# Performance work log

Hardware: AMD Instinct MI355X
Metric: run time of the kernel (lower is better)

The kernel has to match this reference:

```python
import jax, jax.numpy as jnp
import numpy as np

N = 131072       # active sparse sites (fixed)
C_IN = 256       # FPN input channels
HID = 512        # CONV_HEAD_DIM
K = 9            # 3x3 kernel taps
LAYERS = 8       # NUM_STACKED_CONVS
GROUPS = 32      # GroupNorm groups (detectron2 default)
EPS = 1e-5


def _build_rulebook(rng):
    # Sample sparse occupancy over 64 ROIs of 64x64, build 3x3 neighbor map.
    B, H, W = 64, 64, 64
    mask = rng.random((B, H, W)) < 0.60
    coords = np.argwhere(mask)[:N]          # [N,3] (b,y,x), fixed N
    assert coords.shape[0] == N
    grid = -np.ones((B, H + 2, W + 2), np.int32)  # padded, -1 = inactive
    grid[coords[:, 0], coords[:, 1] + 1, coords[:, 2] + 1] = np.arange(N, dtype=np.int32)
    offs = [(dy, dx) for dy in (-1, 0, 1) for dx in (-1, 0, 1)]
    nbr = np.stack(
        [grid[coords[:, 0], coords[:, 1] + 1 + dy, coords[:, 2] + 1 + dx] for dy, dx in offs],
        axis=1,
    )  # [N,9], -1 where neighbor inactive (submanifold: output sites == input sites)
    return nbr


def setup_inputs() -> dict:
    rng = np.random.default_rng(0)
    nbr = _build_rulebook(rng)
    key = jax.random.key(0)
    k0, k1, k2, k3, k4 = jax.random.split(key, 5)
    features = jax.random.normal(k0, (N, C_IN), jnp.float32)
    w0 = jax.random.normal(k1, (K, C_IN, HID), jnp.float32) * (1.0 / np.sqrt(K * C_IN))
    w_rest = jax.random.normal(k2, (LAYERS - 1, K, HID, HID), jnp.float32) * (1.0 / np.sqrt(K * HID))
    gamma = 1.0 + 0.1 * jax.random.normal(k3, (LAYERS, HID), jnp.float32)
    beta = 0.1 * jax.random.normal(k4, (LAYERS, HID), jnp.float32)
    return {
        "features": features,
        "nbr_idx": jnp.asarray(nbr),
        "w0": w0,
        "w_rest": w_rest,
        "gamma": gamma,
        "beta": beta,
    }


def _subm_conv(x, nbr_idx, w):
    # gather-GEMM-scatter submanifold conv: x [N,Cin], nbr_idx [N,K], w [K,Cin,Cout]
    n = x.shape[0]
    xp = jnp.concatenate([x, jnp.zeros((1, x.shape[1]), x.dtype)], axis=0)  # zero row for -1
    idx = jnp.where(nbr_idx < 0, n, nbr_idx)
    out = jnp.zeros((n, w.shape[2]), x.dtype)
    for k in range(K):  # fixed small loop over kernel taps
        out = out + xp[idx[:, k]] @ w[k]
    return out


def _group_norm(x, g, b):
    # per-point GroupNorm over channel groups: x [N,C]
    n, c = x.shape
    xg = x.reshape(n, GROUPS, c // GROUPS)
    mu = jnp.mean(xg, axis=-1, keepdims=True)
    var = jnp.var(xg, axis=-1, keepdims=True)
    xg = (xg - mu) * jax.lax.rsqrt(var + EPS)
    return xg.reshape(n, c) * g + b


def reference(features, nbr_idx, w0, w_rest, gamma, beta):
    x = jax.nn.relu(_group_norm(_subm_conv(features, nbr_idx, w0), gamma[0], beta[0]))
    for i in range(LAYERS - 1):
        x = jax.nn.relu(_group_norm(_subm_conv(x, nbr_idx, w_rest[i]), gamma[i + 1], beta[i + 1]))
    return x
```

## Files before the change

kernel.cpp:

```cpp
#include <hip/hip_runtime.h>
#include <stdint.h>

#define N_SITES 131072
#define CIN0 256
#define HID 512
#define KTAPS 9
#define NLAYERS 8

typedef __bf16 bf16x8 __attribute__((ext_vector_type(8)));
typedef float f32x4 __attribute__((ext_vector_type(4)));

__device__ __forceinline__ unsigned short f2bf(float f) {
    union { float f; unsigned u; } v; v.f = f;
    return (unsigned short)((v.u + 0x7fffu + ((v.u >> 16) & 1u)) >> 16);
}


__global__ void cvt_features_kernel(const float* __restrict__ in, unsigned short* __restrict__ out) {
    int t = blockIdx.x * 256 + threadIdx.x;
    const float4* p = (const float4*)in + 2 * (size_t)t;
    float4 a = p[0], b = p[1];
    uint4 o;
    o.x = f2bf(a.x) | ((unsigned)f2bf(a.y) << 16);
    o.y = f2bf(a.z) | ((unsigned)f2bf(a.w) << 16);
    o.z = f2bf(b.x) | ((unsigned)f2bf(b.y) << 16);
    o.w = f2bf(b.z) | ((unsigned)f2bf(b.w) << 16);
    ((uint4*)out)[t] = o;
}

__global__ void zero_rows_kernel(unsigned short* __restrict__ xf, unsigned short* __restrict__ xo) {
    int t = threadIdx.x;
    xf[(size_t)N_SITES * 512 + t] = 0;
    xf[(size_t)N_SITES * 512 + 256 + t] = 0;
    xo[(size_t)N_SITES * 256 + t] = 0;
    xo[(size_t)N_SITES * 512 + t] = 0;
    xo[(size_t)N_SITES * 512 + 256 + t] = 0;
}

__global__ void transpose_w_kernel(const float* __restrict__ in, unsigned short* __restrict__ out, int cin) {
    __shared__ float tile[32][33];
    int m = blockIdx.z;
    int nb = blockIdx.x * 32;
    int cb = blockIdx.y * 32;
    int tx = threadIdx.x, ty = threadIdx.y;
    const float* src = in + (size_t)m * cin * HID;
    unsigned short* dst = out + (size_t)m * HID * cin;
#pragma unroll
    for (int j = 0; j < 4; ++j) {
        int r = ty + 8 * j;
        tile[r][tx] = src[(size_t)(cb + r) * HID + nb + tx];
    }
    __syncthreads();
#pragma unroll
    for (int j = 0; j < 4; ++j) {
        int r = ty + 8 * j;
        dst[(size_t)(nb + r) * cin + cb + tx] = f2bf(tile[tx][r]);
    }
}


__device__ __forceinline__ void async16(const void* g, void* l) {
    __builtin_amdgcn_global_load_lds(
        (__attribute__((address_space(1))) unsigned int*)(g),
        (__attribute__((address_space(3))) unsigned int*)(l),
        16, 0, 0);
}

__global__ __launch_bounds__(256, 4) void subm_gemm_gn_kernel(
    const unsigned short* __restrict__ x,
    const int* __restrict__ nbr,
    const unsigned short* __restrict__ wt,
    const float* __restrict__ gamma,
    const float* __restrict__ beta,
    void* __restrict__ obuf,
    int cin, int write_bf16)
{
    __shared__ uint4 As[1024];
    __shared__ uint4 Bs[1024];

    const int tid = threadIdx.x;
    const int lane = tid & 63;
    const int wave = tid >> 6;

    const int b = (int)blockIdx.x;
    const int xcd = b & 7;
    const int slot = b >> 3;
    const int colbase = (xcd & 3) * 128;
    const int rowbase = ((xcd >> 2) * 512 + slot) * 128;

    const int wm = (wave >> 1) * 64;
    const int wn = (wave & 1) * 64;

    const int r0 = tid >> 3;
    const int cs = tid & 7;
    const int chunk = cs ^ (r0 & 7);
    const int ldsbase = tid & ~63;
    const int kiters = cin >> 6;

    const f32x4 zero4 = {0.f, 0.f, 0.f, 0.f};
    f32x4 acc[4][4];
#pragma unroll
    for (int i = 0; i < 4; ++i)
#pragma unroll
        for (int j = 0; j < 4; ++j)
            acc[i][j] = zero4;

    for (int tap = 0; tap < KTAPS; ++tap) {
        const unsigned short* arow[4];
#pragma unroll
        for (int i = 0; i < 4; ++i) {
            int idx = nbr[(size_t)(rowbase + r0 + 32 * i) * KTAPS + tap];
            if (idx < 0) idx = N_SITES;
            arow[i] = x + (size_t)idx * cin + chunk * 8;
        }
        const unsigned short* wbase = wt + ((size_t)tap * HID + colbase) * cin + chunk * 8;
        const unsigned short* brow[4];
#pragma unroll
        for (int i = 0; i < 4; ++i)
            brow[i] = wbase + (size_t)(r0 + 32 * i) * cin;

        for (int kk = 0; kk < kiters; ++kk) {
            const int ko = kk * 64;
            __syncthreads();
#pragma unroll
            for (int i = 0; i < 4; ++i) {
                async16(arow[i] + ko, &As[ldsbase + 256 * i]);
                async16(brow[i] + ko, &Bs[ldsbase + 256 * i]);
            }
            __syncthreads();

#pragma unroll
            for (int ks = 0; ks < 2; ++ks) {
                bf16x8 af[4], bfr[4];
#pragma unroll
                for (int f = 0; f < 4; ++f) {
                    int rl = wm + f * 16 + (lane & 15);
                    int ch = ks * 4 + (lane >> 4);
                    af[f]  = __builtin_bit_cast(bf16x8, As[rl * 8 + (ch ^ (rl & 7))]);
                    int cl = wn + f * 16 + (lane & 15);
                    bfr[f] = __builtin_bit_cast(bf16x8, Bs[cl * 8 + (ch ^ (cl & 7))]);
                }
#pragma unroll
                for (int i = 0; i < 4; ++i)
#pragma unroll
                    for (int j = 0; j < 4; ++j)
                        acc[i][j] = __builtin_amdgcn_mfma_f32_16x16x32_bf16(af[i], bfr[j], acc[i][j], 0, 0, 0);
            }
        }
    }

    float gv[4], bv[4];
#pragma unroll
    for (int j = 0; j < 4; ++j) {
        int gcol = colbase + wn + j * 16 + (lane & 15);
        gv[j] = gamma[gcol];
        bv[j] = beta[gcol];
    }

    unsigned short* bf_out = (unsigned short*)obuf;
    float* f_out = (float*)obuf;

#pragma unroll
    for (int i = 0; i < 4; ++i) {
        const int grow = rowbase + wm + i * 16 + (lane >> 4) * 4;
#pragma unroll
        for (int j = 0; j < 4; ++j) {
            const int gcol = colbase + wn + j * 16 + (lane & 15);
            f32x4 v = acc[i][j];
            f32x4 s = v;
            f32x4 q = v * v;
#pragma unroll
            for (int m = 1; m < 16; m <<= 1) {
#pragma unroll
                for (int r = 0; r < 4; ++r) {
                    s[r] += __shfl_xor(s[r], m);
                    q[r] += __shfl_xor(q[r], m);
                }
            }
            f32x4 y;
#pragma unroll
            for (int r = 0; r < 4; ++r) {
                float mu = s[r] * 0.0625f;
                float rstd = rsqrtf(q[r] * 0.0625f - mu * mu + 1e-5f);
                y[r] = fmaxf(0.f, (v[r] - mu) * rstd * gv[j] + bv[j]);
            }
            if (write_bf16) {
#pragma unroll
                for (int r = 0; r < 4; ++r)
                    bf_out[(size_t)(grow + r) * HID + gcol] = f2bf(y[r]);
            } else {
#pragma unroll
                for (int r = 0; r < 4; ++r)
                    f_out[(size_t)(grow + r) * HID + gcol] = y[r];
            }
        }
    }
}


extern "C" void kernel_launch(void* const* d_in, const int* in_sizes, int n_in,
                              void* d_out, int out_size, void* d_ws, size_t ws_size,
                              hipStream_t stream) {
    const float* features = (const float*)d_in[0];
    const int*   nbr      = (const int*)d_in[1];
    const float* w0       = (const float*)d_in[2];
    const float* w_rest   = (const float*)d_in[3];
    const float* gamma    = (const float*)d_in[4];
    const float* beta     = (const float*)d_in[5];

    unsigned short* xF = (unsigned short*)d_ws;
    size_t xbytes = (size_t)(N_SITES + 1) * HID * sizeof(unsigned short);
    unsigned short* w0t = (unsigned short*)((char*)d_ws + xbytes);
    size_t w0t_bytes = (size_t)KTAPS * HID * CIN0 * sizeof(unsigned short);
    unsigned short* wrt = (unsigned short*)((char*)d_ws + xbytes + w0t_bytes);
    unsigned short* xO = (unsigned short*)d_out;

    cvt_features_kernel<<<N_SITES * CIN0 / (256 * 8), 256, 0, stream>>>(features, xO);
    zero_rows_kernel<<<1, 256, 0, stream>>>(xF, xO);
    transpose_w_kernel<<<dim3(HID / 32, CIN0 / 32, KTAPS), dim3(32, 8), 0, stream>>>(w0, w0t, CIN0);
    transpose_w_kernel<<<dim3(HID / 32, HID / 32, (NLAYERS - 1) * KTAPS), dim3(32, 8), 0, stream>>>(w_rest, wrt, HID);

    for (int l = 0; l < NLAYERS; ++l) {
        const unsigned short* wt = (l == 0) ? w0t : wrt + (size_t)(l - 1) * KTAPS * HID * HID;
        int cin = (l == 0) ? CIN0 : HID;
        const unsigned short* xin = (l & 1) ? xF : xO;
        void* obuf = (l == NLAYERS - 1) ? d_out : (void*)((l & 1) ? xO : xF);
        subm_gemm_gn_kernel<<<(N_SITES / 128) * 4, 256, 0, stream>>>(
            xin, nbr, wt, gamma + (size_t)l * HID, beta + (size_t)l * HID,
            obuf, cin, (l < NLAYERS - 1) ? 1 : 0);
    }
}
```

Measured before the change: 5.314 ms.

## Use 256x256 tiles with double-buffered eight-phase MFMA pipeline and LDS epilogue

Replaces the 128x128-tile, single-buffered gather-GEMM kernel with a 512-thread, 256x256-tile kernel templated on input channels. Global-to-LDS async loads of the next k-slice are interleaved with MFMA phases under explicit vmcnt waits, barriers and s_setprio. The kernel caches neighbor indices in shared memory and routes the GroupNorm epilogue through LDS so stores are vectorized. This aims to hide gather latency and raise per-block data reuse. In exchange it uses more registers and LDS and lowers occupancy, which risks spills or fewer resident waves.

```diff
diff --git a/kernel.cpp b/kernel.cpp
--- a/kernel.cpp
+++ b/kernel.cpp
@@ -66,132 +66,240 @@
         16, 0, 0);
 }
 
-__global__ __launch_bounds__(256, 4) void subm_gemm_gn_kernel(
+#define BARRIER() do { asm volatile("" ::: "memory"); __builtin_amdgcn_s_barrier(); asm volatile("" ::: "memory"); } while (0)
+#define WAIT_LGKM0() asm volatile("s_waitcnt lgkmcnt(0)" ::: "memory")
+#define WAIT_VM4() asm volatile("s_waitcnt vmcnt(4)" ::: "memory")
+#define WAIT_VM0() asm volatile("s_waitcnt vmcnt(0)" ::: "memory")
+
+#define MFMA4(I, A, B0_, B1_, B2_, B3_) \
+    acc[I][0] = __builtin_amdgcn_mfma_f32_16x16x32_bf16(A, B0_, acc[I][0], 0, 0, 0); \
+    acc[I][1] = __builtin_amdgcn_mfma_f32_16x16x32_bf16(A, B1_, acc[I][1], 0, 0, 0); \
+    acc[I][2] = __builtin_amdgcn_mfma_f32_16x16x32_bf16(A, B2_, acc[I][2], 0, 0, 0); \
+    acc[I][3] = __builtin_amdgcn_mfma_f32_16x16x32_bf16(A, B3_, acc[I][3], 0, 0, 0);
+
+template<int CIN>
+__global__ __launch_bounds__(512, 2) void subm_gemm_gn_8ph(
     const unsigned short* __restrict__ x,
     const int* __restrict__ nbr,
     const unsigned short* __restrict__ wt,
     const float* __restrict__ gamma,
     const float* __restrict__ beta,
     void* __restrict__ obuf,
-    int cin, int write_bf16)
+    int write_bf16)
 {
-    __shared__ uint4 As[1024];
-    __shared__ uint4 Bs[1024];
+    constexpr int KK = CIN / 64;
+    __shared__ uint4 lds[8192];
+    __shared__ int nbrS[256 * KTAPS];
 
     const int tid = threadIdx.x;
     const int lane = tid & 63;
     const int wave = tid >> 6;
+    const int wm = (wave >> 2) * 128;
+    const int wn = (wave & 3) * 64;
 
     const int b = (int)blockIdx.x;
     const int xcd = b & 7;
     const int slot = b >> 3;
-    const int colbase = (xcd & 3) * 128;
-    const int rowbase = ((xcd >> 2) * 512 + slot) * 128;
-
-    const int wm = (wave >> 1) * 64;
-    const int wn = (wave & 1) * 64;
-
-    const int r0 = tid >> 3;
-    const int cs = tid & 7;
-    const int chunk = cs ^ (r0 & 7);
-    const int ldsbase = tid & ~63;
-    const int kiters = cin >> 6;
+    const int colbase = (xcd & 1) * 256;
+    const int rowbase = ((xcd >> 1) * 128 + slot) * 256;
+
+    const int srow = 2 * (tid >> 3) + ((tid >> 2) & 1);
+    const int scl = (tid & 3) ^ ((tid >> 3) & 3);
+    const int ldsw = tid & ~63;
+
+    for (int u = tid; u < 256 * KTAPS; u += 512) {
+        int v = nbr[(size_t)rowbase * KTAPS + u];
+        nbrS[u] = (v < 0) ? N_SITES : v;
+    }
+    __syncthreads();
 
     const f32x4 zero4 = {0.f, 0.f, 0.f, 0.f};
-    f32x4 acc[4][4];
-#pragma unroll
-    for (int i = 0; i < 4; ++i)
+    f32x4 acc[8][4];
+#pragma unroll
+    for (int i = 0; i < 8; ++i)
 #pragma unroll
         for (int j = 0; j < 4; ++j)
             acc[i][j] = zero4;
 
+    auto stageA = [&](int i0, int i1, int kkp, int kh, int buf) {
+        const unsigned short* g0 = x + (size_t)i0 * CIN + kkp * 64 + kh * 32 + scl * 8;
+        const unsigned short* g1 = x + (size_t)i1 * CIN + kkp * 64 + kh * 32 + scl * 8;
+        async16(g0, &lds[buf * 4096 + kh * 1024 + ldsw]);
+        async16(g1, &lds[buf * 4096 + kh * 1024 + 512 + ldsw]);
+    };
+    auto stageB = [&](int tp, int kkp, int kh, int buf) {
+        const unsigned short* g0 = wt + (size_t)(tp * HID + colbase + srow) * CIN + kkp * 64 + kh * 32 + scl * 8;
+        const unsigned short* g1 = wt + (size_t)(tp * HID + colbase + srow + 128) * CIN + kkp * 64 + kh * 32 + scl * 8;
+        async16(g0, &lds[buf * 4096 + 2048 + kh * 1024 + ldsw]);
+        async16(g1, &lds[buf * 4096 + 2048 + kh * 1024 + 512 + ldsw]);
+    };
+    auto rdA = [&](int i, int ks, int buf) {
+        int rl = wm + i * 16 + (lane & 15);
+        return __builtin_bit_cast(bf16x8,
+            lds[buf * 4096 + ks * 1024 + (rl >> 1) * 8 + (rl & 1) * 4 + ((lane >> 4) ^ ((rl >> 1) & 3))]);
+    };
+    auto rdB = [&](int j, int ks, int buf) {
+        int rn = wn + j * 16 + (lane & 15);
+        return __builtin_bit_cast(bf16x8,
+            lds[buf * 4096 + 2048 + ks * 1024 + (rn >> 1) * 8 + (rn & 1) * 4 + ((lane >> 4) ^ ((rn >> 1) & 3))]);
+    };
+
+    {
+        int a0 = nbrS[srow * KTAPS], a1 = nbrS[(srow + 128) * KTAPS];
+        stageA(a0, a1, 0, 0, 0);
+        stageB(0, 0, 0, 0);
+        stageA(a0, a1, 0, 1, 0);
+        stageB(0, 0, 1, 0);
+    }
+    WAIT_VM4();
+    BARRIER();
+
     for (int tap = 0; tap < KTAPS; ++tap) {
-        const unsigned short* arow[4];
-#pragma unroll
-        for (int i = 0; i < 4; ++i) {
-            int idx = nbr[(size_t)(rowbase + r0 + 32 * i) * KTAPS + tap];
-            if (idx < 0) idx = N_SITES;
-            arow[i] = x + (size_t)idx * cin + chunk * 8;
+#pragma unroll 2
+        for (int kk = 0; kk < KK; ++kk) {
+            const int p = kk & 1;
+            const int q = p ^ 1;
+            const bool haveNext = !(tap == KTAPS - 1 && kk == KK - 1);
+            const int ntap = (kk == KK - 1) ? tap + 1 : tap;
+            const int nkk = (kk == KK - 1) ? 0 : kk + 1;
+            int nA0 = 0, nA1 = 0;
+            if (haveNext) {
+                nA0 = nbrS[srow * KTAPS + ntap];
+                nA1 = nbrS[(srow + 128) * KTAPS + ntap];
+            }
+            if (haveNext) stageA(nA0, nA1, nkk, 0, q);
+            bf16x8 a0 = rdA(0, 0, p), a1 = rdA(1, 0, p), a2 = rdA(2, 0, p), a3 = rdA(3, 0, p);
+            bf16x8 b0 = rdB(0, 0, p), b1 = rdB(1, 0, p), b2 = rdB(2, 0, p), b3 = rdB(3, 0, p);
+            BARRIER();
+            WAIT_LGKM0();
+            __builtin_amdgcn_s_setprio(1);
+            MFMA4(0, a0, b0, b1, b2, b3)
+            MFMA4(1, a1, b0, b1, b2, b3)
+            MFMA4(2, a2, b0, b1, b2, b3)
+            MFMA4(3, a3, b0, b1, b2, b3)
+            __builtin_amdgcn_s_setprio(0);
+            BARRIER();
+            if (haveNext) stageB(ntap, nkk, 0, q);
+            {
+                bf16x8 a4 = rdA(4, 0, p), a5 = rdA(5, 0, p), a6 = rdA(6, 0, p), a7 = rdA(7, 0, p);
+                BARRIER();
+                WAIT_LGKM0();
+                __builtin_amdgcn_s_setprio(1);
+                MFMA4(4, a4, b0, b1, b2, b3)
+                MFMA4(5, a5, b0, b1, b2, b3)
+                MFMA4(6, a6, b0, b1, b2, b3)
+                MFMA4(7, a7, b0, b1, b2, b3)
+                __builtin_amdgcn_s_setprio(0);
+            }
+            if (haveNext) { WAIT_VM4(); } else { WAIT_VM0(); }
+            BARRIER();
+            if (haveNext) stageA(nA0, nA1, nkk, 1, q);
+            a0 = rdA(0, 1, p); a1 = rdA(1, 1, p); a2 = rdA(2, 1, p); a3 = rdA(3, 1, p);
+            b0 = rdB(0, 1, p); b1 = rdB(1, 1, p); b2 = rdB(2, 1, p); b3 = rdB(3, 1, p);
+            BARRIER();
+            WAIT_LGKM0();
+            __builtin_amdgcn_s_setprio(1);
+            MFMA4(0, a0, b0, b1, b2, b3)
+            MFMA4(1, a1, b0, b1, b2, b3)
+            MFMA4(2, a2, b0, b1, b2, b3)
+            MFMA4(3, a3, b0, b1, b2, b3)
+            __builtin_amdgcn_s_setprio(0);
+            BARRIER();
+            if (haveNext) stageB(ntap, nkk, 1, q);
+            {
+                bf16x8 a4 = rdA(4, 1, p), a5 = rdA(5, 1, p), a6 = rdA(6, 1, p), a7 = rdA(7, 1, p);
+                BARRIER();
+                WAIT_LGKM0();
+                __builtin_amdgcn_s_setprio(1);
+                MFMA4(4, a4, b0, b1, b2, b3)
+                MFMA4(5, a5, b0, b1, b2, b3)
+                MFMA4(6, a6, b0, b1, b2, b3)
+                MFMA4(7, a7, b0, b1, b2, b3)
+                __builtin_amdgcn_s_setprio(0);
+            }
+            WAIT_VM4();
+            BARRIER();
         }
-        const unsigned short* wbase = wt + ((size_t)tap * HID + colbase) * cin + chunk * 8;
-        const unsigned short* brow[4];
-#pragma unroll
-        for (int i = 0; i < 4; ++i)
-            brow[i] = wbase + (size_t)(r0 + 32 * i) * cin;
-
-        for (int kk = 0; kk < kiters; ++kk) {
-            const int ko = kk * 64;
-            __syncthreads();
-#pragma unroll
-            for (int i = 0; i < 4; ++i) {
-                async16(arow[i] + ko, &As[ldsbase + 256 * i]);
-                async16(brow[i] + ko, &Bs[ldsbase + 256 * i]);
-            }
-            __syncthreads();
-
-#pragma unroll
-            for (int ks = 0; ks < 2; ++ks) {
-                bf16x8 af[4], bfr[4];
-#pragma unroll
-                for (int f = 0; f < 4; ++f) {
-                    int rl = wm + f * 16 + (lane & 15);
-                    int ch = ks * 4 + (lane >> 4);
-                    af[f]  = __builtin_bit_cast(bf16x8, As[rl * 8 + (ch ^ (rl & 7))]);
-                    int cl = wn + f * 16 + (lane & 15);
-                    bfr[f] = __builtin_bit_cast(bf16x8, Bs[cl * 8 + (ch ^ (cl & 7))]);
-                }
-#pragma unroll
-                for (int i = 0; i < 4; ++i)
-#pragma unroll
-                    for (int j = 0; j < 4; ++j)
-                        acc[i][j] = __builtin_amdgcn_mfma_f32_16x16x32_bf16(af[i], bfr[j], acc[i][j], 0, 0, 0);
-            }
-        }
-    }
-
-    float gv[4], bv[4];
-#pragma unroll
-    for (int j = 0; j < 4; ++j) {
-        int gcol = colbase + wn + j * 16 + (lane & 15);
-        gv[j] = gamma[gcol];
-        bv[j] = beta[gcol];
-    }
-
+    }
+
+    __syncthreads();
+    float* E = (float*)lds;
+    const int seg = tid & 31;
+    const int qv = tid >> 5;
+    const int c0s = seg * 8;
     unsigned short* bf_out = (unsigned short*)obuf;
     float* f_out = (float*)obuf;
 
-#pragma unroll
-    for (int i = 0; i < 4; ++i) {
-        const int grow = rowbase + wm + i * 16 + (lane >> 4) * 4;
-#pragma unroll
-        for (int j = 0; j < 4; ++j) {
-            const int gcol = colbase + wn + j * 16 + (lane & 15);
-            f32x4 v = acc[i][j];
-            f32x4 s = v;
-            f32x4 q = v * v;
-#pragma unroll
-            for (int m = 1; m < 16; m <<= 1) {
+    float gv[8], bv[8];
+#pragma unroll
+    for (int k = 0; k < 8; ++k) {
+        gv[k] = gamma[colbase + c0s + k];
+        bv[k] = beta[colbase + c0s + k];
+    }
+
+#pragma unroll
+    for (int pass = 0; pass < 2; ++pass) {
+        if (pass) __syncthreads();
+#pragma unroll
+        for (int ii = 0; ii < 4; ++ii) {
+#pragma unroll
+            for (int j = 0; j < 4; ++j) {
+                const int col = wn + j * 16 + (lane & 15);
+                const int lrow = (wm >> 1) + ii * 16 + (lane >> 4) * 4;
+                *(f32x4*)&E[col * 128 + (lrow ^ (((col >> 3) & 7) << 2))] = acc[pass * 4 + ii][j];
+            }
+        }
+        __syncthreads();
+#pragma unroll
+        for (int h = 0; h < 2; ++h) {
+            const int r0w = (qv + h * 16) * 4;
+            f32x4 vv[8];
+            f32x4 s = zero4, q2 = zero4;
+#pragma unroll
+            for (int cc = 0; cc < 8; ++cc) {
+                const int col = c0s + cc;
+                vv[cc] = *(const f32x4*)&E[col * 128 + (r0w ^ (((col >> 3) & 7) << 2))];
+                s += vv[cc];
+                q2 += vv[cc] * vv[cc];
+            }
+            f32x4 mu, rs;
+#pragma unroll
+            for (int r = 0; r < 4; ++r) {
+                s[r] += __shfl_xor(s[r], 1);
+                q2[r] += __shfl_xor(q2[r], 1);
+                mu[r] = s[r] * 0.0625f;
+                rs[r] = rsqrtf(q2[r] * 0.0625f - mu[r] * mu[r] + 1e-5f);
+            }
+            if (write_bf16) {
 #pragma unroll
                 for (int r = 0; r < 4; ++r) {
-                    s[r] += __shfl_xor(s[r], m);
-                    q[r] += __shfl_xor(q[r], m);
+                    const int l = r0w + r;
+                    const int grow = rowbase + 64 * pass + (l & 63) + ((l >> 6) << 7);
+                    unsigned pk[4];
+#pragma unroll
+                    for (int cp = 0; cp < 4; ++cp) {
+                        float ya = fmaxf(0.f, (vv[2 * cp][r] - mu[r]) * rs[r] * gv[2 * cp] + bv[2 * cp]);
+                        float yb = fmaxf(0.f, (vv[2 * cp + 1][r] - mu[r]) * rs[r] * gv[2 * cp + 1] + bv[2 * cp + 1]);
+                        pk[cp] = f2bf(ya) | ((unsigned)f2bf(yb) << 16);
+                    }
+                    uint4 o; o.x = pk[0]; o.y = pk[1]; o.z = pk[2]; o.w = pk[3];
+                    *(uint4*)&bf_out[(size_t)grow * HID + colbase + c0s] = o;
                 }
-            }
-            f32x4 y;
-#pragma unroll
-            for (int r = 0; r < 4; ++r) {
-                float mu = s[r] * 0.0625f;
-                float rstd = rsqrtf(q[r] * 0.0625f - mu * mu + 1e-5f);
-                y[r] = fmaxf(0.f, (v[r] - mu) * rstd * gv[j] + bv[j]);
-            }
-            if (write_bf16) {
-#pragma unroll
-                for (int r = 0; r < 4; ++r)
-                    bf_out[(size_t)(grow + r) * HID + gcol] = f2bf(y[r]);
             } else {
 #pragma unroll
-                for (int r = 0; r < 4; ++r)
-                    f_out[(size_t)(grow + r) * HID + gcol] = y[r];
+                for (int r = 0; r < 4; ++r) {
+                    const int l = r0w + r;
+                    const int grow = rowbase + 64 * pass + (l & 63) + ((l >> 6) << 7);
+                    f32x4 ya, yb;
+#pragma unroll
+                    for (int k = 0; k < 4; ++k) {
+                        ya[k] = fmaxf(0.f, (vv[k][r] - mu[r]) * rs[r] * gv[k] + bv[k]);
+                        yb[k] = fmaxf(0.f, (vv[4 + k][r] - mu[r]) * rs[r] * gv[4 + k] + bv[4 + k]);
+                    }
+                    float* dst = f_out + (size_t)grow * HID + colbase + c0s;
+                    *(f32x4*)dst = ya;
+                    *(f32x4*)(dst + 4) = yb;
+                }
             }
         }
     }
@@ -222,11 +330,14 @@
 
     for (int l = 0; l < NLAYERS; ++l) {
         const unsigned short* wt = (l == 0) ? w0t : wrt + (size_t)(l - 1) * KTAPS * HID * HID;
-        int cin = (l == 0) ? CIN0 : HID;
         const unsigned short* xin = (l & 1) ? xF : xO;
         void* obuf = (l == NLAYERS - 1) ? d_out : (void*)((l & 1) ? xO : xF);
-        subm_gemm_gn_kernel<<<(N_SITES / 128) * 4, 256, 0, stream>>>(
-            xin, nbr, wt, gamma + (size_t)l * HID, beta + (size_t)l * HID,
-            obuf, cin, (l < NLAYERS - 1) ? 1 : 0);
-    }
-}
+        const float* g = gamma + (size_t)l * HID;
+        const float* bt = beta + (size_t)l * HID;
+        int wb = (l < NLAYERS - 1) ? 1 : 0;
+        if (l == 0)
+            subm_gemm_gn_8ph<CIN0><<<(N_SITES / 256) * 2, 512, 0, stream>>>(xin, nbr, wt, g, bt, obuf, wb);
+        else
+            subm_gemm_gn_8ph<HID><<<(N_SITES / 256) * 2, 512, 0, stream>>>(xin, nbr, wt, g, bt, obuf, wb);
+    }
+}
```

Result: no change. 5.352 ms (+0.7%).
